# Kernel optimization log

Hardware: AMD Instinct MI355X
Metric: run time of the kernel (lower is better)

## Reference

```python
import jax, jax.numpy as jnp
import numpy as np

N_NODES = 100000
IN_CH = 64
HID = 16
HEADS = 4
OUT_CH = 1
NEG_SLOPE = 0.2
EPS = 1e-16


def gat_conv(x, src, dst, W, att_src, att_dst, bias, heads, out_ch, concat):
    """PyG-style GATConv. src/dst already include self-loops.
    x: [N, F_in]; W: [F_in, heads*out_ch]; att_*: [heads, out_ch]; bias: [heads*out_ch] or [out_ch]."""
    n = x.shape[0]
    h = (x @ W).reshape(n, heads, out_ch)                     # [N,H,C]
    a_src = jnp.einsum('nhc,hc->nh', h, att_src)              # [N,H]
    a_dst = jnp.einsum('nhc,hc->nh', h, att_dst)              # [N,H]
    alpha = jax.nn.leaky_relu(a_src[src] + a_dst[dst], NEG_SLOPE)  # [E,H]
    # segment softmax over incoming edges of each destination node
    m = jax.ops.segment_max(alpha, dst, num_segments=n)       # [N,H]
    e = jnp.exp(alpha - m[dst])
    denom = jax.ops.segment_sum(e, dst, num_segments=n)
    alpha = e / (denom[dst] + EPS)                            # [E,H]
    msg = h[src] * alpha[:, :, None]                          # [E,H,C]
    out = jax.ops.segment_sum(msg, dst, num_segments=n)       # [N,H,C]
    out = out.reshape(n, heads * out_ch) if concat else out.mean(axis=1)
    return out + bias


def setup_inputs() -> dict:
    key = jax.random.key(0)
    ks = jax.random.split(key, 10)
    x = jax.random.normal(ks[0], (N_NODES, IN_CH), dtype=jnp.float32)
    edge_index = jax.random.randint(ks[1], (2, 1600000), 0, N_NODES, dtype=jnp.int64)
    s = 0.1
    W1 = jax.random.normal(ks[2], (IN_CH, HEADS * HID), dtype=jnp.float32) * s
    att_src1 = jax.random.normal(ks[3], (HEADS, HID), dtype=jnp.float32) * s
    att_dst1 = jax.random.normal(ks[4], (HEADS, HID), dtype=jnp.float32) * s
    b1 = jnp.zeros((HEADS * HID,), dtype=jnp.float32)
    W2 = jax.random.normal(ks[5], (HEADS * HID, OUT_CH), dtype=jnp.float32) * s
    att_src2 = jax.random.normal(ks[6], (1, OUT_CH), dtype=jnp.float32) * s
    att_dst2 = jax.random.normal(ks[7], (1, OUT_CH), dtype=jnp.float32) * s
    b2 = jnp.zeros((OUT_CH,), dtype=jnp.float32)
    return {"x": x, "edge_index": edge_index, "W1": W1, "att_src1": att_src1,
            "att_dst1": att_dst1, "b1": b1, "W2": W2, "att_src2": att_src2,
            "att_dst2": att_dst2, "b2": b2}


def reference(x, edge_index, W1, att_src1, att_dst1, b1, W2, att_src2, att_dst2, b2):
    n = x.shape[0]
    loop = jnp.arange(n, dtype=edge_index.dtype)
    src = jnp.concatenate([edge_index[0], loop])  # self-loops (PyG default)
    dst = jnp.concatenate([edge_index[1], loop])
    h = gat_conv(x, src, dst, W1, att_src1, att_dst1, b1, HEADS, HID, concat=True)
    h = jax.nn.elu(h)
    out = gat_conv(h, src, dst, W2, att_src2, att_dst2, b2, 1, OUT_CH, concat=False)
    return out.squeeze()
```

## Files before the change

### kernel.cpp

```cpp
#include <hip/hip_runtime.h>
#include <hip/hip_fp16.h>

#define NN   100000
#define E0   1600000
#define ET   1700000
#define NEG  0.2f
#define EPSV 1e-16f
#define NBK  1563
#define CAP  1536
#define BS   1024
#define NBLK4 ((ET + 4 * BS - 1) / (4 * BS))
#define GEMM_NB 782
#define BC_NB   416
#define E1_NB   6256

typedef _Float16 half8 __attribute__((ext_vector_type(8)));
typedef float f32x16 __attribute__((ext_vector_type(16)));

__global__ __launch_bounds__(256) void k_g1bc(
    const float* __restrict__ x, const int* __restrict__ ei,
    const float* __restrict__ W1, const float* __restrict__ as1,
    const float* __restrict__ ad1,
    __half* __restrict__ h1h, float* __restrict__ asr, float* __restrict__ adr,
    int* __restrict__ bcnt)
{
    int t = threadIdx.x;
    if (blockIdx.x >= GEMM_NB) {
        __shared__ int cnt[NBK];
        for (int i = t; i < NBK; i += 256) cnt[i] = 0;
        __syncthreads();
        int base = (blockIdx.x - GEMM_NB) * (256 * 16);
#pragma unroll
        for (int k = 0; k < 16; ++k) {
            int idx = base + k * 256 + t;
            if (idx < ET) {
                int d = (idx < E0) ? ei[E0 + idx] : (idx - E0);
                atomicAdd(&cnt[d >> 6], 1);
            }
        }
        __syncthreads();
        for (int i = t; i < NBK; i += 256) if (cnt[i]) atomicAdd(&bcnt[i], cnt[i]);
        return;
    }
    __shared__ float Wl[4096];
    __shared__ float Ul[512];
    for (int i = t; i < 4096; i += 256) Wl[i] = W1[i];
    __syncthreads();
    if (t < 64) {
        int k = t;
#pragma unroll
        for (int h = 0; h < 4; ++h) {
            float su = 0.f, du = 0.f;
#pragma unroll
            for (int c = 0; c < 16; ++c) {
                float w = Wl[k * 64 + h * 16 + c];
                su += w * as1[h * 16 + c];
                du += w * ad1[h * 16 + c];
            }
            Ul[k * 8 + h] = su;
            Ul[k * 8 + 4 + h] = du;
        }
    }
    __syncthreads();
    int lane = t & 63, wv = t >> 6;
    int col = lane & 31, q = lane >> 5;
    half8 bf0[4], bf1[4], bf2[4];
#pragma unroll
    for (int kc = 0; kc < 4; ++kc) {
#pragma unroll
        for (int j = 0; j < 8; ++j) {
            int k = kc * 16 + q * 8 + j;
            bf0[kc][j] = (_Float16)Wl[k * 64 + col];
            bf1[kc][j] = (_Float16)Wl[k * 64 + 32 + col];
            bf2[kc][j] = (col < 8) ? (_Float16)Ul[k * 8 + col] : (_Float16)0.f;
        }
    }
    int tile = blockIdx.x * 4 + wv;
    int n0 = tile * 32;
    if (n0 >= NN) return;
    half8 af[4];
    const float* xrow = x + (size_t)(n0 + col) * 64;
#pragma unroll
    for (int kc = 0; kc < 4; ++kc) {
        float4 xa = *(const float4*)(xrow + kc * 16 + q * 8);
        float4 xb = *(const float4*)(xrow + kc * 16 + q * 8 + 4);
        af[kc][0] = (_Float16)xa.x; af[kc][1] = (_Float16)xa.y;
        af[kc][2] = (_Float16)xa.z; af[kc][3] = (_Float16)xa.w;
        af[kc][4] = (_Float16)xb.x; af[kc][5] = (_Float16)xb.y;
        af[kc][6] = (_Float16)xb.z; af[kc][7] = (_Float16)xb.w;
    }
    f32x16 c0 = {}, c1 = {}, c2 = {};
#pragma unroll
    for (int kc = 0; kc < 4; ++kc) {
        c0 = __builtin_amdgcn_mfma_f32_32x32x16_f16(af[kc], bf0[kc], c0, 0, 0, 0);
        c1 = __builtin_amdgcn_mfma_f32_32x32x16_f16(af[kc], bf1[kc], c1, 0, 0, 0);
        c2 = __builtin_amdgcn_mfma_f32_32x32x16_f16(af[kc], bf2[kc], c2, 0, 0, 0);
    }
    int hA = col >> 4, cc = col & 15;
#pragma unroll
    for (int reg = 0; reg < 16; ++reg) {
        int row = (reg & 3) + 8 * (reg >> 2) + 4 * q;
        size_t n = (size_t)(n0 + row);
        h1h[((size_t)hA * NN + n) * 16 + cc]       = __float2half(c0[reg]);
        h1h[((size_t)(hA + 2) * NN + n) * 16 + cc] = __float2half(c1[reg]);
    }
    if (col < 8) {
        float* dst = (col < 4) ? asr : adr;
        int h = col & 3;
#pragma unroll
        for (int reg = 0; reg < 16; ++reg) {
            int row = (reg & 3) + 8 * (reg >> 2) + 4 * q;
            dst[(n0 + row) * 4 + h] = c2[reg];
        }
    }
}

__global__ __launch_bounds__(1024) void k_bscan(const int* __restrict__ bcnt,
                                                int* __restrict__ bbase, int* __restrict__ bcursor)
{
    int t = threadIdx.x;
    int i0 = 2 * t, i1 = 2 * t + 1;
    int a = (i0 < NBK) ? bcnt[i0] : 0;
    int b = (i1 < NBK) ? bcnt[i1] : 0;
    int s = a + b;
    int lane = t & 63, wid = t >> 6;
    int sc = s;
#pragma unroll
    for (int off = 1; off < 64; off <<= 1) {
        int u = __shfl_up(sc, off, 64);
        if (lane >= off) sc += u;
    }
    __shared__ int wsum[16];
    if (lane == 63) wsum[wid] = sc;
    __syncthreads();
    int woff = 0;
    for (int k = 0; k < wid; ++k) woff += wsum[k];
    int excl = sc - s + woff;
    if (i0 < NBK) { bbase[i0] = excl;     bcursor[i0] = excl; }
    if (i1 < NBK) { bbase[i1] = excl + a; bcursor[i1] = excl + a; }
}

__global__ __launch_bounds__(BS) void k_bscat(const int* __restrict__ ei,
                                              int* __restrict__ bcursor, int* __restrict__ bin)
{
    __shared__ int cnt[NBK];
    __shared__ int base[NBK];
    int t = threadIdx.x;
    for (int i = t; i < NBK; i += BS) cnt[i] = 0;
    __syncthreads();
    int blk = blockIdx.x * (BS * 4);
    int b[4], r[4], pk[4];
#pragma unroll
    for (int k = 0; k < 4; ++k) {
        int idx = blk + k * BS + t;
        r[k] = -1;
        if (idx < ET) {
            int s, d;
            if (idx < E0) { s = ei[idx]; d = ei[E0 + idx]; } else { s = d = idx - E0; }
            b[k] = d >> 6;
            pk[k] = s | ((d & 63) << 17);
            r[k] = atomicAdd(&cnt[b[k]], 1);
        }
    }
    __syncthreads();
    for (int i = t; i < NBK; i += BS) if (cnt[i]) base[i] = atomicAdd(&bcursor[i], cnt[i]);
    __syncthreads();
#pragma unroll
    for (int k = 0; k < 4; ++k)
        if (r[k] >= 0) bin[base[b[k]] + r[k]] = pk[k];
}

__global__ __launch_bounds__(256) void k_bsort(
    int* __restrict__ bin, const int* __restrict__ bbase, const int* __restrict__ bcnt,
    const float* __restrict__ asr, const float* __restrict__ adr,
    int* __restrict__ binH1, int* __restrict__ binH2, int* __restrict__ binH3,
    int* __restrict__ A)
{
    __shared__ int raw[CAP];
    __shared__ float adl[256];
    __shared__ int deg[64], cur[64];
    int b = blockIdx.x, t = threadIdx.x;
    int beg = bbase[b], cnt = bcnt[b];
    if (cnt > CAP) cnt = CAP;
    if (t < 64) deg[t] = 0;
    {
        int gi = b * 256 + t;
        adl[t] = (gi < NN * 4) ? adr[gi] : 0.f;
    }
    for (int i = t; i < cnt; i += 256) raw[i] = bin[beg + i];
    __syncthreads();
    for (int i = t; i < cnt; i += 256) atomicAdd(&deg[raw[i] >> 17], 1);
    __syncthreads();
    if (t < 64) {
        int v = deg[t];
        int sc = v;
#pragma unroll
        for (int off = 1; off < 64; off <<= 1) {
            int u = __shfl_up(sc, off, 64);
            if (t >= off) sc += u;
        }
        cur[t] = sc - v;
        int n = b * 64 + t;
        if (n < NN) A[n] = beg + sc;
    }
    __syncthreads();
    for (int i = t; i < cnt; i += 256) {
        int e = raw[i];
        int s = e & 0x1FFFF, dl = e >> 17;
        float4 as4 = *(const float4*)(asr + s * 4);
        int dl4 = dl * 4;
        float a0 = as4.x + adl[dl4 + 0]; a0 = a0 > 0.f ? a0 : NEG * a0;
        float a1 = as4.y + adl[dl4 + 1]; a1 = a1 > 0.f ? a1 : NEG * a1;
        float a2 = as4.z + adl[dl4 + 2]; a2 = a2 > 0.f ? a2 : NEG * a2;
        float a3 = as4.w + adl[dl4 + 3]; a3 = a3 > 0.f ? a3 : NEG * a3;
        int q0 = (int)__half_as_ushort(__float2half(__expf(a0)));
        int q1 = (int)__half_as_ushort(__float2half(__expf(a1)));
        int q2 = (int)__half_as_ushort(__float2half(__expf(a2)));
        int q3 = (int)__half_as_ushort(__float2half(__expf(a3)));
        int r = atomicAdd(&cur[dl], 1);
        int gp = beg + r;
        bin[gp]   = s | (q0 << 17);
        binH1[gp] = s | (q1 << 17);
        binH2[gp] = s | (q2 << 17);
        binH3[gp] = s | (q3 << 17);
    }
}

__global__ __launch_bounds__(256) void k_e1agg(
    const int* __restrict__ binH0, const int* __restrict__ binH1,
    const int* __restrict__ binH2, const int* __restrict__ binH3,
    const int* __restrict__ A,
    const int* __restrict__ bbase, const int* __restrict__ bcnt,
    const __half* __restrict__ h1h,
    const float* __restrict__ b1, const float* __restrict__ W2,
    float* __restrict__ g)
{
    __shared__ int lw[CAP];
    int bid = blockIdx.x, t = threadIdx.x;
    int lane8 = bid & 7;
    int h = lane8 >> 1;
    int b = (bid >> 3) * 2 + (lane8 & 1);
    if (b >= NBK) return;
    int beg = bbase[b], cnt = bcnt[b];
    if (cnt > CAP) cnt = CAP;
    const int* bh = (h == 0) ? binH0 : (h == 1) ? binH1 : (h == 2) ? binH2 : binH3;
    for (int i = t; i < cnt; i += 256) lw[i] = bh[beg + i];
    __syncthreads();
    int q = t & 3, nl = t >> 2;
    int n = b * 64 + nl;
    if (n >= NN) return;
    int je = A[n] - beg;               if (je > cnt) je = cnt;
    int jb = ((n == 0) ? 0 : A[n - 1]) - beg; if (jb < 0) jb = 0;
    size_t hb = (size_t)h * NN;
    int p = q & 1, eo = q >> 1;
    float acc[8];
#pragma unroll
    for (int c = 0; c < 8; ++c) acc[c] = 0.f;
    float den = 0.f;
    for (int e = jb + eo; e < je; e += 2) {
        int w = lw[e];
        int s = w & 0x1FFFF;
        float evf = __half2float(__ushort_as_half((unsigned short)((unsigned)w >> 17)));
        den += evf;
        uint4 r0 = *(const uint4*)(h1h + (hb + s) * 16 + p * 8);
        float2 f0 = __half22float2(*(const __half2*)&r0.x);
        float2 f1 = __half22float2(*(const __half2*)&r0.y);
        float2 f2 = __half22float2(*(const __half2*)&r0.z);
        float2 f3 = __half22float2(*(const __half2*)&r0.w);
        acc[0] += evf * f0.x; acc[1] += evf * f0.y;
        acc[2] += evf * f1.x; acc[3] += evf * f1.y;
        acc[4] += evf * f2.x; acc[5] += evf * f2.y;
        acc[6] += evf * f3.x; acc[7] += evf * f3.y;
    }
#pragma unroll
    for (int c = 0; c < 8; ++c) acc[c] += __shfl_xor(acc[c], 2);
    den += __shfl_xor(den, 2);
    float inv = 1.f / (den + EPSV);
    const float* bp = b1 + h * 16 + p * 8;
    const float* wp = W2 + h * 16 + p * 8;
    float gv = 0.f;
#pragma unroll
    for (int c = 0; c < 8; ++c) {
        float v = acc[c] * inv + bp[c];
        v = v > 0.f ? v : __expf(v) - 1.f;
        gv += v * wp[c];
    }
    gv += __shfl_xor(gv, 1);
    if (q == 0) atomicAdd(&g[n], gv);
}

__global__ __launch_bounds__(256) void k_e2agg(
    const int* __restrict__ binH0, const int* __restrict__ A,
    const int* __restrict__ bbase, const int* __restrict__ bcnt,
    const float* __restrict__ g, const float* __restrict__ as2,
    const float* __restrict__ ad2, const float* __restrict__ b2,
    float* __restrict__ out)
{
    __shared__ int lcsr[CAP];
    int b = blockIdx.x, t = threadIdx.x;
    int beg = bbase[b], cnt = bcnt[b];
    if (cnt > CAP) cnt = CAP;
    for (int i = t; i < cnt; i += 256) lcsr[i] = binH0[beg + i] & 0x1FFFF;
    __syncthreads();
    int p = t & 3, nl = t >> 2;
    int n = b * 64 + nl;
    if (n >= NN) return;
    int je = A[n] - beg;               if (je > cnt) je = cnt;
    int jb = ((n == 0) ? 0 : A[n - 1]) - beg; if (jb < 0) jb = 0;
    float cs = as2[0];
    float gdcd = g[n] * ad2[0];
    float acc = 0.f, den = 0.f;
    for (int j = jb + p; j < je; j += 4) {
        float gz = g[lcsr[j]];
        float a = gz * cs + gdcd;
        a = a > 0.f ? a : NEG * a;
        float ev = __expf(a);
        den += ev;
        acc += ev * gz;
    }
    acc += __shfl_xor(acc, 1); den += __shfl_xor(den, 1);
    acc += __shfl_xor(acc, 2); den += __shfl_xor(den, 2);
    if (p == 0) out[n] = acc / (den + EPSV) + b2[0];
}

extern "C" void kernel_launch(void* const* d_in, const int* in_sizes, int n_in,
                              void* d_out, int out_size, void* d_ws, size_t ws_size,
                              hipStream_t stream)
{
    const float* x   = (const float*)d_in[0];
    const int*   ei  = (const int*)d_in[1];
    const float* W1  = (const float*)d_in[2];
    const float* as1 = (const float*)d_in[3];
    const float* ad1 = (const float*)d_in[4];
    const float* b1  = (const float*)d_in[5];
    const float* W2  = (const float*)d_in[6];
    const float* as2 = (const float*)d_in[7];
    const float* ad2 = (const float*)d_in[8];
    const float* b2  = (const float*)d_in[9];
    float* out = (float*)d_out;

    int*   iw      = (int*)d_ws;
    float* fw      = (float*)d_ws;
    int*   bcnt    = iw;
    int*   bbase   = iw + 1664;
    int*   bcursor = iw + 3328;
    int*   A       = iw + 4992;
    int*   bin     = iw + 105344;
    int*   binH1   = iw + 1805344;
    int*   binH2   = iw + 3505344;
    int*   binH3   = iw + 5205344;
    float* asr     = fw + 6905344;
    float* adr     = fw + 7305344;
    float* g       = fw + 7705344;
    __half* h1hQ   = (__half*)(fw + 7805376);

    hipMemsetAsync(bcnt, 0, NBK * sizeof(int), stream);
    hipMemsetAsync(g, 0, NN * sizeof(float), stream);

    k_g1bc  <<<GEMM_NB + BC_NB, 256, 0, stream>>>(x, ei, W1, as1, ad1,
                                                  h1hQ, asr, adr, bcnt);
    k_bscan <<<1, 1024, 0, stream>>>(bcnt, bbase, bcursor);
    k_bscat <<<NBLK4, BS, 0, stream>>>(ei, bcursor, bin);
    k_bsort <<<NBK, 256, 0, stream>>>(bin, bbase, bcnt, asr, adr,
                                      binH1, binH2, binH3, A);
    k_e1agg <<<E1_NB, 256, 0, stream>>>(bin, binH1, binH2, binH3, A, bbase, bcnt,
                                        h1hQ, b1, W2, g);
    k_e2agg <<<NBK, 256, 0, stream>>>(bin, A, bbase, bcnt, g, as2, ad2, b2, out);
}
```

Before: 224.6 us.

## Move edge attention exp from bin sort into aggregation, store head-major scores

The bin sort kernel no longer computes per-edge attention exponentials or writes four per-head packed edge arrays. It now only sorts source indices through shared memory and writes a single coalesced array. The layer-1 aggregation recomputes leaky-relu and exp per edge from head-major src/dst score arrays, and both aggregation loops are unrolled by two to overlap gathers. This removes about 3x1.7M int writes and the matching reads, at the cost of an extra scattered float gather and exp per edge per head in the aggregation, and it drops the fp16 quantisation of the exponentials.

After: 221.8 us. Within noise of the previous version (-1.2%).

```diff
diff --git a/kernel.cpp b/kernel.cpp
--- a/kernel.cpp
+++ b/kernel.cpp
@@ -21,7 +21,7 @@
     const float* __restrict__ x, const int* __restrict__ ei,
     const float* __restrict__ W1, const float* __restrict__ as1,
     const float* __restrict__ ad1,
-    __half* __restrict__ h1h, float* __restrict__ asr, float* __restrict__ adr,
+    __half* __restrict__ h1h, float* __restrict__ asrcm, float* __restrict__ adrm,
     int* __restrict__ bcnt)
 {
     int t = threadIdx.x;
@@ -105,12 +105,12 @@
         h1h[((size_t)(hA + 2) * NN + n) * 16 + cc] = __float2half(c1[reg]);
     }
     if (col < 8) {
-        float* dst = (col < 4) ? asr : adr;
+        float* dst = (col < 4) ? asrcm : adrm;
         int h = col & 3;
 #pragma unroll
         for (int reg = 0; reg < 16; ++reg) {
             int row = (reg & 3) + 8 * (reg >> 2) + 4 * q;
-            dst[(n0 + row) * 4 + h] = c2[reg];
+            dst[(size_t)h * NN + (n0 + row)] = c2[reg];
         }
     }
 }
@@ -172,21 +172,15 @@
 
 __global__ __launch_bounds__(256) void k_bsort(
     int* __restrict__ bin, const int* __restrict__ bbase, const int* __restrict__ bcnt,
-    const float* __restrict__ asr, const float* __restrict__ adr,
-    int* __restrict__ binH1, int* __restrict__ binH2, int* __restrict__ binH3,
     int* __restrict__ A)
 {
     __shared__ int raw[CAP];
-    __shared__ float adl[256];
+    __shared__ int srt[CAP];
     __shared__ int deg[64], cur[64];
     int b = blockIdx.x, t = threadIdx.x;
     int beg = bbase[b], cnt = bcnt[b];
     if (cnt > CAP) cnt = CAP;
     if (t < 64) deg[t] = 0;
-    {
-        int gi = b * 256 + t;
-        adl[t] = (gi < NN * 4) ? adr[gi] : 0.f;
-    }
     for (int i = t; i < cnt; i += 256) raw[i] = bin[beg + i];
     __syncthreads();
     for (int i = t; i < cnt; i += 256) atomicAdd(&deg[raw[i] >> 17], 1);
@@ -206,31 +200,17 @@
     __syncthreads();
     for (int i = t; i < cnt; i += 256) {
         int e = raw[i];
-        int s = e & 0x1FFFF, dl = e >> 17;
-        float4 as4 = *(const float4*)(asr + s * 4);
-        int dl4 = dl * 4;
-        float a0 = as4.x + adl[dl4 + 0]; a0 = a0 > 0.f ? a0 : NEG * a0;
-        float a1 = as4.y + adl[dl4 + 1]; a1 = a1 > 0.f ? a1 : NEG * a1;
-        float a2 = as4.z + adl[dl4 + 2]; a2 = a2 > 0.f ? a2 : NEG * a2;
-        float a3 = as4.w + adl[dl4 + 3]; a3 = a3 > 0.f ? a3 : NEG * a3;
-        int q0 = (int)__half_as_ushort(__float2half(__expf(a0)));
-        int q1 = (int)__half_as_ushort(__float2half(__expf(a1)));
-        int q2 = (int)__half_as_ushort(__float2half(__expf(a2)));
-        int q3 = (int)__half_as_ushort(__float2half(__expf(a3)));
-        int r = atomicAdd(&cur[dl], 1);
-        int gp = beg + r;
-        bin[gp]   = s | (q0 << 17);
-        binH1[gp] = s | (q1 << 17);
-        binH2[gp] = s | (q2 << 17);
-        binH3[gp] = s | (q3 << 17);
-    }
+        int r = atomicAdd(&cur[e >> 17], 1);
+        srt[r] = e & 0x1FFFF;
+    }
+    __syncthreads();
+    for (int i = t; i < cnt; i += 256) bin[beg + i] = srt[i];
 }
 
 __global__ __launch_bounds__(256) void k_e1agg(
-    const int* __restrict__ binH0, const int* __restrict__ binH1,
-    const int* __restrict__ binH2, const int* __restrict__ binH3,
-    const int* __restrict__ A,
+    const int* __restrict__ bin, const int* __restrict__ A,
     const int* __restrict__ bbase, const int* __restrict__ bcnt,
+    const float* __restrict__ asrcm, const float* __restrict__ adrm,
     const __half* __restrict__ h1h,
     const float* __restrict__ b1, const float* __restrict__ W2,
     float* __restrict__ g)
@@ -243,8 +223,7 @@
     if (b >= NBK) return;
     int beg = bbase[b], cnt = bcnt[b];
     if (cnt > CAP) cnt = CAP;
-    const int* bh = (h == 0) ? binH0 : (h == 1) ? binH1 : (h == 2) ? binH2 : binH3;
-    for (int i = t; i < cnt; i += 256) lw[i] = bh[beg + i];
+    for (int i = t; i < cnt; i += 256) lw[i] = bin[beg + i];
     __syncthreads();
     int q = t & 3, nl = t >> 2;
     int n = b * 64 + nl;
@@ -253,25 +232,42 @@
     int jb = ((n == 0) ? 0 : A[n - 1]) - beg; if (jb < 0) jb = 0;
     size_t hb = (size_t)h * NN;
     int p = q & 1, eo = q >> 1;
+    float adv = adrm[hb + n];
     float acc[8];
 #pragma unroll
     for (int c = 0; c < 8; ++c) acc[c] = 0.f;
     float den = 0.f;
-    for (int e = jb + eo; e < je; e += 2) {
-        int w = lw[e];
-        int s = w & 0x1FFFF;
-        float evf = __half2float(__ushort_as_half((unsigned short)((unsigned)w >> 17)));
-        den += evf;
-        uint4 r0 = *(const uint4*)(h1h + (hb + s) * 16 + p * 8);
-        float2 f0 = __half22float2(*(const __half2*)&r0.x);
-        float2 f1 = __half22float2(*(const __half2*)&r0.y);
-        float2 f2 = __half22float2(*(const __half2*)&r0.z);
-        float2 f3 = __half22float2(*(const __half2*)&r0.w);
-        acc[0] += evf * f0.x; acc[1] += evf * f0.y;
-        acc[2] += evf * f1.x; acc[3] += evf * f1.y;
-        acc[4] += evf * f2.x; acc[5] += evf * f2.y;
-        acc[6] += evf * f3.x; acc[7] += evf * f3.y;
-    }
+
+#define ACC1(avv, rr) { \
+        float a = avv + adv; a = a > 0.f ? a : NEG * a; \
+        float ev = __expf(a); den += ev; \
+        float2 f0 = __half22float2(*(const __half2*)&rr.x); \
+        float2 f1 = __half22float2(*(const __half2*)&rr.y); \
+        float2 f2 = __half22float2(*(const __half2*)&rr.z); \
+        float2 f3 = __half22float2(*(const __half2*)&rr.w); \
+        acc[0] += ev * f0.x; acc[1] += ev * f0.y; \
+        acc[2] += ev * f1.x; acc[3] += ev * f1.y; \
+        acc[4] += ev * f2.x; acc[5] += ev * f2.y; \
+        acc[6] += ev * f3.x; acc[7] += ev * f3.y; }
+
+    int e = jb + eo;
+    for (; e + 2 < je; e += 4) {
+        int s0 = lw[e], s1 = lw[e + 2];
+        float av0 = asrcm[hb + s0];
+        float av1 = asrcm[hb + s1];
+        uint4 r0 = *(const uint4*)(h1h + (hb + s0) * 16 + p * 8);
+        uint4 r1 = *(const uint4*)(h1h + (hb + s1) * 16 + p * 8);
+        ACC1(av0, r0)
+        ACC1(av1, r1)
+    }
+    if (e < je) {
+        int s0 = lw[e];
+        float av0 = asrcm[hb + s0];
+        uint4 r0 = *(const uint4*)(h1h + (hb + s0) * 16 + p * 8);
+        ACC1(av0, r0)
+    }
+#undef ACC1
+
 #pragma unroll
     for (int c = 0; c < 8; ++c) acc[c] += __shfl_xor(acc[c], 2);
     den += __shfl_xor(den, 2);
@@ -290,7 +286,7 @@
 }
 
 __global__ __launch_bounds__(256) void k_e2agg(
-    const int* __restrict__ binH0, const int* __restrict__ A,
+    const int* __restrict__ bin, const int* __restrict__ A,
     const int* __restrict__ bbase, const int* __restrict__ bcnt,
     const float* __restrict__ g, const float* __restrict__ as2,
     const float* __restrict__ ad2, const float* __restrict__ b2,
@@ -300,7 +296,7 @@
     int b = blockIdx.x, t = threadIdx.x;
     int beg = bbase[b], cnt = bcnt[b];
     if (cnt > CAP) cnt = CAP;
-    for (int i = t; i < cnt; i += 256) lcsr[i] = binH0[beg + i] & 0x1FFFF;
+    for (int i = t; i < cnt; i += 256) lcsr[i] = bin[beg + i];
     __syncthreads();
     int p = t & 3, nl = t >> 2;
     int n = b * 64 + nl;
@@ -310,14 +306,24 @@
     float cs = as2[0];
     float gdcd = g[n] * ad2[0];
     float acc = 0.f, den = 0.f;
-    for (int j = jb + p; j < je; j += 4) {
-        float gz = g[lcsr[j]];
-        float a = gz * cs + gdcd;
-        a = a > 0.f ? a : NEG * a;
-        float ev = __expf(a);
-        den += ev;
-        acc += ev * gz;
-    }
+
+#define ACC2(gz) { \
+        float a = gz * cs + gdcd; a = a > 0.f ? a : NEG * a; \
+        float ev = __expf(a); den += ev; acc += ev * gz; }
+
+    int j = jb + p;
+    for (; j + 4 < je; j += 8) {
+        int s0 = lcsr[j], s1 = lcsr[j + 4];
+        float g0 = g[s0], g1 = g[s1];
+        ACC2(g0)
+        ACC2(g1)
+    }
+    if (j < je) {
+        float g0 = g[lcsr[j]];
+        ACC2(g0)
+    }
+#undef ACC2
+
     acc += __shfl_xor(acc, 1); den += __shfl_xor(den, 1);
     acc += __shfl_xor(acc, 2); den += __shfl_xor(den, 2);
     if (p == 0) out[n] = acc / (den + EPSV) + b2[0];
@@ -346,24 +352,20 @@
     int*   bcursor = iw + 3328;
     int*   A       = iw + 4992;
     int*   bin     = iw + 105344;
-    int*   binH1   = iw + 1805344;
-    int*   binH2   = iw + 3505344;
-    int*   binH3   = iw + 5205344;
-    float* asr     = fw + 6905344;
-    float* adr     = fw + 7305344;
-    float* g       = fw + 7705344;
-    __half* h1hQ   = (__half*)(fw + 7805376);
+    float* asrcm   = fw + 1805344;
+    float* adrm    = fw + 2205344;
+    float* g       = fw + 2605344;
+    __half* h1hQ   = (__half*)(fw + 2705376);
 
     hipMemsetAsync(bcnt, 0, NBK * sizeof(int), stream);
     hipMemsetAsync(g, 0, NN * sizeof(float), stream);
 
     k_g1bc  <<<GEMM_NB + BC_NB, 256, 0, stream>>>(x, ei, W1, as1, ad1,
-                                                  h1hQ, asr, adr, bcnt);
+                                                  h1hQ, asrcm, adrm, bcnt);
     k_bscan <<<1, 1024, 0, stream>>>(bcnt, bbase, bcursor);
     k_bscat <<<NBLK4, BS, 0, stream>>>(ei, bcursor, bin);
-    k_bsort <<<NBK, 256, 0, stream>>>(bin, bbase, bcnt, asr, adr,
-                                      binH1, binH2, binH3, A);
-    k_e1agg <<<E1_NB, 256, 0, stream>>>(bin, binH1, binH2, binH3, A, bbase, bcnt,
+    k_bsort <<<NBK, 256, 0, stream>>>(bin, bbase, bcnt, A);
+    k_e1agg <<<E1_NB, 256, 0, stream>>>(bin, A, bbase, bcnt, asrcm, adrm,
                                         h1hQ, b1, W2, g);
     k_e2agg <<<NBK, 256, 0, stream>>>(bin, A, bbase, bcnt, g, as2, ad2, b2, out);
 }
```
